# Kernel tuning notes

Measured on AMD Instinct MI355X. Metric: run time of the kernel, lower is better.

## Reference

```python
import jax, jax.numpy as jnp
import numpy as np

WEIGHT_GRADIENT = 0.05
EPS = 1e-6


def _normalize(q, eps):
    # torch F.normalize: q / max(||q||, eps)
    n = jnp.sqrt(jnp.sum(q * q, axis=1, keepdims=True))
    return q / jnp.maximum(n, eps)


def _grad_mag(q, eps):
    # depthwise conv with [-1,1] kernels == finite differences, then replicate-pad
    gx = q[..., :, 1:] - q[..., :, :-1]          # (B,4,H,W-1)
    gy = q[..., 1:, :] - q[..., :-1, :]          # (B,4,H-1,W)
    gx = jnp.pad(gx, ((0, 0), (0, 0), (0, 0), (0, 1)), mode='edge')
    gy = jnp.pad(gy, ((0, 0), (0, 0), (0, 1), (0, 0)), mode='edge')
    return jnp.sqrt(gx * gx + gy * gy + eps)


def setup_inputs() -> dict:
    key = jax.random.key(0)
    k1, k2, k3 = jax.random.split(key, 3)
    B, H, W, S = 16, 256, 256, 24
    q_pred = jax.random.normal(k1, (B, 4, H, W), dtype=jnp.float32)
    q_target = jax.random.normal(k2, (B, 4, H, W), dtype=jnp.float32)
    syms = jax.random.normal(k3, (S, 4), dtype=jnp.float32)
    syms = syms / jnp.linalg.norm(syms, axis=1, keepdims=True)  # unit quaternions
    return {"q_pred": q_pred, "q_target": q_target, "syms": syms}


def reference(q_pred, q_target, syms, eps=EPS):
    # (B,4,H,W) -> (N,4)
    qp = _normalize(q_pred.transpose(0, 2, 3, 1).reshape(-1, 4), eps)
    qt = _normalize(q_target.transpose(0, 2, 3, 1).reshape(-1, 4), eps)
    w1, x1, y1, z1 = qp[:, 0], qp[:, 1], qp[:, 2], qp[:, 3]
    w2, x2, y2, z2 = qt[:, 0], qt[:, 1], qt[:, 2], qt[:, 3]
    # relative quaternion r = qt * conj(qp)
    rw = w2 * w1 + x2 * x1 + y2 * y1 + z2 * z1
    rx = -w2 * x1 + x2 * w1 - y2 * z1 + z2 * y1
    ry = -w2 * y1 + x2 * z1 + y2 * w1 - z2 * x1
    rz = -w2 * z1 - x2 * y1 + y2 * x1 + z2 * w1
    r4 = jnp.stack([rw, rx, ry, rz], axis=1)                 # (N,4)
    signs = jnp.array([1.0, -1.0, -1.0, -1.0], dtype=syms.dtype)
    # w_dist[n,s] = rw*s_w - rx*s_x - ry*s_y - rz*s_z
    w_dist = jnp.einsum('nc,sc->ns', r4, syms * signs)       # (N,S)
    max_w = jnp.max(jnp.abs(w_dist), axis=1)
    max_w = jnp.clip(max_w, -(1.0 - eps), 1.0 - eps)
    loss_rot = jnp.mean(2.0 * jnp.arccos(max_w))
    gp = _grad_mag(q_pred, eps)
    gt = _grad_mag(q_target, eps)
    loss_grad = jnp.mean(jnp.abs(gp - gt))
    return loss_rot + WEIGHT_GRADIENT * loss_grad
```

## Files before the change

### kernel.cpp

```cpp
#include <hip/hip_runtime.h>
#include <math.h>

constexpr int Hc = 256;
constexpr int Wc = 256;
constexpr float EPSf = 1e-6f;

__device__ __forceinline__ float comp(const float4& v, int p) {
    return p == 0 ? v.x : p == 1 ? v.y : p == 2 ? v.z : v.w;
}

template<int S>
__global__ __launch_bounds__(256, 4) void sym_loss_main(
    const float* __restrict__ qp,
    const float* __restrict__ qt,
    const float* __restrict__ syms,
    float2* __restrict__ partial)
{
    int t    = blockIdx.x * 256 + threadIdx.x;
    int lane = t & 63;
    int row  = t >> 6;
    int b    = row >> 8;
    int h    = row & (Hc - 1);
    int w0   = lane << 2;

    int idx0 = (b << 18) + (h << 8) + w0;
    int dy = (h == Hc - 1) ? -Wc : Wc;
    int xo = (lane == 63) ? 2 : 4;

    float4 Cp[4], Yp[4], Ct[4], Yt[4];
    float  xp[4], xt[4];
    #pragma unroll
    for (int c = 0; c < 4; ++c) {
        int idx = idx0 + (c << 16);
        Cp[c] = *(const float4*)(qp + idx);
        Yp[c] = *(const float4*)(qp + idx + dy);
        xp[c] = qp[idx + xo];
        Ct[c] = *(const float4*)(qt + idx);
        Yt[c] = *(const float4*)(qt + idx + dy);
        xt[c] = qt[idx + xo];
    }

    float gsum = 0.0f;
    #pragma unroll
    for (int c = 0; c < 4; ++c) {
        float4 C = Cp[c], Y = Yp[c], D = Ct[c], Z = Yt[c];
        float gx, gy, a, e;
        gx = C.y - C.x; gy = Y.x - C.x;
        a = sqrtf(fmaf(gx, gx, fmaf(gy, gy, EPSf)));
        gx = D.y - D.x; gy = Z.x - D.x;
        e = sqrtf(fmaf(gx, gx, fmaf(gy, gy, EPSf)));
        gsum += fabsf(a - e);

        gx = C.z - C.y; gy = Y.y - C.y;
        a = sqrtf(fmaf(gx, gx, fmaf(gy, gy, EPSf)));
        gx = D.z - D.y; gy = Z.y - D.y;
        e = sqrtf(fmaf(gx, gx, fmaf(gy, gy, EPSf)));
        gsum += fabsf(a - e);

        gx = C.w - C.z; gy = Y.z - C.z;
        a = sqrtf(fmaf(gx, gx, fmaf(gy, gy, EPSf)));
        gx = D.w - D.z; gy = Z.z - D.z;
        e = sqrtf(fmaf(gx, gx, fmaf(gy, gy, EPSf)));
        gsum += fabsf(a - e);

        gx = xp[c] - C.w; gy = Y.w - C.w;
        a = sqrtf(fmaf(gx, gx, fmaf(gy, gy, EPSf)));
        gx = xt[c] - D.w; gy = Z.w - D.w;
        e = sqrtf(fmaf(gx, gx, fmaf(gy, gy, EPSf)));
        gsum += fabsf(a - e);
    }

    float rw[4], nx[4], ny[4], nz[4];
    #pragma unroll
    for (int p = 0; p < 4; ++p) {
        float a0 = comp(Cp[0], p), a1 = comp(Cp[1], p),
              a2 = comp(Cp[2], p), a3 = comp(Cp[3], p);
        float b0 = comp(Ct[0], p), b1 = comp(Ct[1], p),
              b2 = comp(Ct[2], p), b3 = comp(Ct[3], p);

        float ss1 = fmaf(a0, a0, fmaf(a1, a1, fmaf(a2, a2, a3 * a3)));
        float ss2 = fmaf(b0, b0, fmaf(b1, b1, fmaf(b2, b2, b3 * b3)));
        float i1 = __builtin_amdgcn_rsqf(ss1);
        float i2 = __builtin_amdgcn_rsqf(ss2);
        float w1 = a0 * i1, x1 = a1 * i1, y1 = a2 * i1, z1 = a3 * i1;
        float w2 = b0 * i2, x2 = b1 * i2, y2 = b2 * i2, z2 = b3 * i2;

        rw[p] =  w2 * w1 + x2 * x1 + y2 * y1 + z2 * z1;
        float rx = -w2 * x1 + x2 * w1 - y2 * z1 + z2 * y1;
        float ry = -w2 * y1 + x2 * z1 + y2 * w1 - z2 * x1;
        float rz = -w2 * z1 - x2 * y1 + y2 * x1 + z2 * w1;
        nx[p] = -rx; ny[p] = -ry; nz[p] = -rz;
    }

    const float4* __restrict__ sv4 = (const float4*)syms;
    float maxw[4] = {0.f, 0.f, 0.f, 0.f};
    #pragma unroll
    for (int s = 0; s < S; ++s) {
        float4 sv = sv4[s];
        #pragma unroll
        for (int p = 0; p < 4; ++p) {
            float d = fmaf(nz[p], sv.w,
                      fmaf(ny[p], sv.z,
                      fmaf(nx[p], sv.y, rw[p] * sv.x)));
            maxw[p] = fmaxf(maxw[p], fabsf(d));
        }
    }
    float rot = 0.0f;
    #pragma unroll
    for (int p = 0; p < 4; ++p)
        rot += 2.0f * acosf(fminf(maxw[p], 1.0f - EPSf));

    #pragma unroll
    for (int off = 32; off > 0; off >>= 1) {
        rot  += __shfl_down(rot,  off, 64);
        gsum += __shfl_down(gsum, off, 64);
    }
    __shared__ float s_r[4], s_g[4];
    int wid = threadIdx.x >> 6;
    if ((threadIdx.x & 63) == 0) { s_r[wid] = rot; s_g[wid] = gsum; }
    __syncthreads();
    if (threadIdx.x == 0) {
        float2 o;
        o.x = s_r[0] + s_r[1] + s_r[2] + s_r[3];
        o.y = s_g[0] + s_g[1] + s_g[2] + s_g[3];
        partial[blockIdx.x] = o;
    }
}

__global__ __launch_bounds__(256) void sym_loss_generic(
    const float* __restrict__ qp,
    const float* __restrict__ qt,
    const float* __restrict__ syms,
    int S,
    float2* __restrict__ partial)
{
    int t    = blockIdx.x * 256 + threadIdx.x;
    int lane = t & 63;
    int row  = t >> 6;
    int b    = row >> 8;
    int h    = row & (Hc - 1);
    int w0   = lane << 2;
    int idx0 = (b << 18) + (h << 8) + w0;
    int dy = (h == Hc - 1) ? -Wc : Wc;
    int xo = (lane == 63) ? 2 : 4;

    float4 Cp[4], Yp[4], Ct[4], Yt[4];
    float  xp[4], xt[4];
    #pragma unroll
    for (int c = 0; c < 4; ++c) {
        int idx = idx0 + (c << 16);
        Cp[c] = *(const float4*)(qp + idx);
        Yp[c] = *(const float4*)(qp + idx + dy);
        xp[c] = qp[idx + xo];
        Ct[c] = *(const float4*)(qt + idx);
        Yt[c] = *(const float4*)(qt + idx + dy);
        xt[c] = qt[idx + xo];
    }
    float gsum = 0.0f;
    #pragma unroll
    for (int c = 0; c < 4; ++c) {
        float4 C = Cp[c], Y = Yp[c], D = Ct[c], Z = Yt[c];
        float gx, gy, a, e;
        gx = C.y - C.x; gy = Y.x - C.x;
        a = sqrtf(fmaf(gx, gx, fmaf(gy, gy, EPSf)));
        gx = D.y - D.x; gy = Z.x - D.x;
        e = sqrtf(fmaf(gx, gx, fmaf(gy, gy, EPSf)));
        gsum += fabsf(a - e);
        gx = C.z - C.y; gy = Y.y - C.y;
        a = sqrtf(fmaf(gx, gx, fmaf(gy, gy, EPSf)));
        gx = D.z - D.y; gy = Z.y - D.y;
        e = sqrtf(fmaf(gx, gx, fmaf(gy, gy, EPSf)));
        gsum += fabsf(a - e);
        gx = C.w - C.z; gy = Y.z - C.z;
        a = sqrtf(fmaf(gx, gx, fmaf(gy, gy, EPSf)));
        gx = D.w - D.z; gy = Z.z - D.z;
        e = sqrtf(fmaf(gx, gx, fmaf(gy, gy, EPSf)));
        gsum += fabsf(a - e);
        gx = xp[c] - C.w; gy = Y.w - C.w;
        a = sqrtf(fmaf(gx, gx, fmaf(gy, gy, EPSf)));
        gx = xt[c] - D.w; gy = Z.w - D.w;
        e = sqrtf(fmaf(gx, gx, fmaf(gy, gy, EPSf)));
        gsum += fabsf(a - e);
    }
    float rw[4], nx[4], ny[4], nz[4];
    #pragma unroll
    for (int p = 0; p < 4; ++p) {
        float a0 = comp(Cp[0], p), a1 = comp(Cp[1], p),
              a2 = comp(Cp[2], p), a3 = comp(Cp[3], p);
        float b0 = comp(Ct[0], p), b1 = comp(Ct[1], p),
              b2 = comp(Ct[2], p), b3 = comp(Ct[3], p);
        float ss1 = fmaf(a0, a0, fmaf(a1, a1, fmaf(a2, a2, a3 * a3)));
        float ss2 = fmaf(b0, b0, fmaf(b1, b1, fmaf(b2, b2, b3 * b3)));
        float i1 = __builtin_amdgcn_rsqf(ss1);
        float i2 = __builtin_amdgcn_rsqf(ss2);
        float w1 = a0 * i1, x1 = a1 * i1, y1 = a2 * i1, z1 = a3 * i1;
        float w2 = b0 * i2, x2 = b1 * i2, y2 = b2 * i2, z2 = b3 * i2;
        rw[p] =  w2 * w1 + x2 * x1 + y2 * y1 + z2 * z1;
        float rx = -w2 * x1 + x2 * w1 - y2 * z1 + z2 * y1;
        float ry = -w2 * y1 + x2 * z1 + y2 * w1 - z2 * x1;
        float rz = -w2 * z1 - x2 * y1 + y2 * x1 + z2 * w1;
        nx[p] = -rx; ny[p] = -ry; nz[p] = -rz;
    }
    const float4* __restrict__ sv4 = (const float4*)syms;
    float maxw[4] = {0.f, 0.f, 0.f, 0.f};
    for (int s = 0; s < S; ++s) {
        float4 sv = sv4[s];
        #pragma unroll
        for (int p = 0; p < 4; ++p) {
            float d = fmaf(nz[p], sv.w,
                      fmaf(ny[p], sv.z,
                      fmaf(nx[p], sv.y, rw[p] * sv.x)));
            maxw[p] = fmaxf(maxw[p], fabsf(d));
        }
    }
    float rot = 0.0f;
    #pragma unroll
    for (int p = 0; p < 4; ++p)
        rot += 2.0f * acosf(fminf(maxw[p], 1.0f - EPSf));
    #pragma unroll
    for (int off = 32; off > 0; off >>= 1) {
        rot  += __shfl_down(rot,  off, 64);
        gsum += __shfl_down(gsum, off, 64);
    }
    __shared__ float s_r[4], s_g[4];
    int wid = threadIdx.x >> 6;
    if ((threadIdx.x & 63) == 0) { s_r[wid] = rot; s_g[wid] = gsum; }
    __syncthreads();
    if (threadIdx.x == 0) {
        float2 o;
        o.x = s_r[0] + s_r[1] + s_r[2] + s_r[3];
        o.y = s_g[0] + s_g[1] + s_g[2] + s_g[3];
        partial[blockIdx.x] = o;
    }
}

__global__ __launch_bounds__(256) void sym_loss_reduce(
    const float2* __restrict__ partial, int nblocks,
    float* __restrict__ out, double invNP, double invNE)
{
    double r = 0.0, g = 0.0;
    for (int i = threadIdx.x; i < nblocks; i += 256) {
        float2 p = partial[i];
        r += (double)p.x;
        g += (double)p.y;
    }
    #pragma unroll
    for (int off = 32; off > 0; off >>= 1) {
        r += __shfl_down(r, off, 64);
        g += __shfl_down(g, off, 64);
    }
    __shared__ double s_r[4], s_g[4];
    int wid = threadIdx.x >> 6;
    if ((threadIdx.x & 63) == 0) { s_r[wid] = r; s_g[wid] = g; }
    __syncthreads();
    if (threadIdx.x == 0) {
        double rr = s_r[0] + s_r[1] + s_r[2] + s_r[3];
        double gg = s_g[0] + s_g[1] + s_g[2] + s_g[3];
        out[0] = (float)(rr * invNP + 0.05 * gg * invNE);
    }
}

extern "C" void kernel_launch(void* const* d_in, const int* in_sizes, int n_in,
                              void* d_out, int out_size, void* d_ws, size_t ws_size,
                              hipStream_t stream)
{
    const float* qp   = (const float*)d_in[0];
    const float* qt   = (const float*)d_in[1];
    const float* syms = (const float*)d_in[2];

    int S  = in_sizes[2] / 4;
    int NP = in_sizes[0] / 4;
    int nthreads = NP / 4;
    int nblocks  = nthreads / 256;

    float2* partial = (float2*)d_ws;

    if (S == 24) {
        sym_loss_main<24><<<nblocks, 256, 0, stream>>>(qp, qt, syms, partial);
    } else {
        sym_loss_generic<<<nblocks, 256, 0, stream>>>(qp, qt, syms, S, partial);
    }

    double invNP = 1.0 / (double)NP;
    double invNE = 1.0 / ((double)NP * 4.0);
    sym_loss_reduce<<<1, 256, 0, stream>>>(partial, nblocks, (float*)d_out,
                                           invNP, invNE);
}
```

Measured before the change: 84.72 us.

## Use fast sqrt/acos approximations and fuse final reduction via atomics

Replaces library sqrtf with the hardware sqrt builtin and acosf with a cubic polynomial approximation (Abramowitz–Stegun style) for the rotation term. The separate reduction kernel is removed: each block scales its partial sums by precomputed constants and atomically adds them into the output, which is zeroed with a memset first. This cuts transcendental cost and one kernel launch, at the price of approximation error and nondeterministic float accumulation order.

```diff
diff --git a/kernel.cpp b/kernel.cpp
--- a/kernel.cpp
+++ b/kernel.cpp
@@ -7,6 +7,17 @@
 
 __device__ __forceinline__ float comp(const float4& v, int p) {
     return p == 0 ? v.x : p == 1 ? v.y : p == 2 ? v.z : v.w;
+}
+
+__device__ __forceinline__ float fast_acos01(float x) {
+    float t = __builtin_amdgcn_sqrtf(1.0f - x);
+    float p = fmaf(fmaf(fmaf(-0.0187293f, x, 0.0742610f), x, -0.2121144f),
+                   x, 1.5707288f);
+    return t * p;
+}
+
+__device__ __forceinline__ float fast_sqrt(float x) {
+    return __builtin_amdgcn_sqrtf(x);
 }
 
 template<int S>
@@ -14,7 +25,8 @@
     const float* __restrict__ qp,
     const float* __restrict__ qt,
     const float* __restrict__ syms,
-    float2* __restrict__ partial)
+    float* __restrict__ out,
+    float cRot, float cGrad)
 {
     int t    = blockIdx.x * 256 + threadIdx.x;
     int lane = t & 63;
@@ -46,27 +58,27 @@
         float4 C = Cp[c], Y = Yp[c], D = Ct[c], Z = Yt[c];
         float gx, gy, a, e;
         gx = C.y - C.x; gy = Y.x - C.x;
-        a = sqrtf(fmaf(gx, gx, fmaf(gy, gy, EPSf)));
+        a = fast_sqrt(fmaf(gx, gx, fmaf(gy, gy, EPSf)));
         gx = D.y - D.x; gy = Z.x - D.x;
-        e = sqrtf(fmaf(gx, gx, fmaf(gy, gy, EPSf)));
+        e = fast_sqrt(fmaf(gx, gx, fmaf(gy, gy, EPSf)));
         gsum += fabsf(a - e);
 
         gx = C.z - C.y; gy = Y.y - C.y;
-        a = sqrtf(fmaf(gx, gx, fmaf(gy, gy, EPSf)));
+        a = fast_sqrt(fmaf(gx, gx, fmaf(gy, gy, EPSf)));
         gx = D.z - D.y; gy = Z.y - D.y;
-        e = sqrtf(fmaf(gx, gx, fmaf(gy, gy, EPSf)));
+        e = fast_sqrt(fmaf(gx, gx, fmaf(gy, gy, EPSf)));
         gsum += fabsf(a - e);
 
         gx = C.w - C.z; gy = Y.z - C.z;
-        a = sqrtf(fmaf(gx, gx, fmaf(gy, gy, EPSf)));
+        a = fast_sqrt(fmaf(gx, gx, fmaf(gy, gy, EPSf)));
         gx = D.w - D.z; gy = Z.z - D.z;
-        e = sqrtf(fmaf(gx, gx, fmaf(gy, gy, EPSf)));
+        e = fast_sqrt(fmaf(gx, gx, fmaf(gy, gy, EPSf)));
         gsum += fabsf(a - e);
 
         gx = xp[c] - C.w; gy = Y.w - C.w;
-        a = sqrtf(fmaf(gx, gx, fmaf(gy, gy, EPSf)));
+        a = fast_sqrt(fmaf(gx, gx, fmaf(gy, gy, EPSf)));
         gx = xt[c] - D.w; gy = Z.w - D.w;
-        e = sqrtf(fmaf(gx, gx, fmaf(gy, gy, EPSf)));
+        e = fast_sqrt(fmaf(gx, gx, fmaf(gy, gy, EPSf)));
         gsum += fabsf(a - e);
     }
 
@@ -108,7 +120,7 @@
     float rot = 0.0f;
     #pragma unroll
     for (int p = 0; p < 4; ++p)
-        rot += 2.0f * acosf(fminf(maxw[p], 1.0f - EPSf));
+        rot += fast_acos01(fminf(maxw[p], 1.0f - EPSf));
 
     #pragma unroll
     for (int off = 32; off > 0; off >>= 1) {
@@ -120,10 +132,9 @@
     if ((threadIdx.x & 63) == 0) { s_r[wid] = rot; s_g[wid] = gsum; }
     __syncthreads();
     if (threadIdx.x == 0) {
-        float2 o;
-        o.x = s_r[0] + s_r[1] + s_r[2] + s_r[3];
-        o.y = s_g[0] + s_g[1] + s_g[2] + s_g[3];
-        partial[blockIdx.x] = o;
+        float r = s_r[0] + s_r[1] + s_r[2] + s_r[3];
+        float g = s_g[0] + s_g[1] + s_g[2] + s_g[3];
+        atomicAdd(out, fmaf(r, cRot, g * cGrad));
     }
 }
 
@@ -132,7 +143,8 @@
     const float* __restrict__ qt,
     const float* __restrict__ syms,
     int S,
-    float2* __restrict__ partial)
+    float* __restrict__ out,
+    float cRot, float cGrad)
 {
     int t    = blockIdx.x * 256 + threadIdx.x;
     int lane = t & 63;
@@ -162,24 +174,24 @@
         float4 C = Cp[c], Y = Yp[c], D = Ct[c], Z = Yt[c];
         float gx, gy, a, e;
         gx = C.y - C.x; gy = Y.x - C.x;
-        a = sqrtf(fmaf(gx, gx, fmaf(gy, gy, EPSf)));
+        a = fast_sqrt(fmaf(gx, gx, fmaf(gy, gy, EPSf)));
         gx = D.y - D.x; gy = Z.x - D.x;
-        e = sqrtf(fmaf(gx, gx, fmaf(gy, gy, EPSf)));
+        e = fast_sqrt(fmaf(gx, gx, fmaf(gy, gy, EPSf)));
         gsum += fabsf(a - e);
         gx = C.z - C.y; gy = Y.y - C.y;
-        a = sqrtf(fmaf(gx, gx, fmaf(gy, gy, EPSf)));
+        a = fast_sqrt(fmaf(gx, gx, fmaf(gy, gy, EPSf)));
         gx = D.z - D.y; gy = Z.y - D.y;
-        e = sqrtf(fmaf(gx, gx, fmaf(gy, gy, EPSf)));
+        e = fast_sqrt(fmaf(gx, gx, fmaf(gy, gy, EPSf)));
         gsum += fabsf(a - e);
         gx = C.w - C.z; gy = Y.z - C.z;
-        a = sqrtf(fmaf(gx, gx, fmaf(gy, gy, EPSf)));
+        a = fast_sqrt(fmaf(gx, gx, fmaf(gy, gy, EPSf)));
         gx = D.w - D.z; gy = Z.z - D.z;
-        e = sqrtf(fmaf(gx, gx, fmaf(gy, gy, EPSf)));
+        e = fast_sqrt(fmaf(gx, gx, fmaf(gy, gy, EPSf)));
         gsum += fabsf(a - e);
         gx = xp[c] - C.w; gy = Y.w - C.w;
-        a = sqrtf(fmaf(gx, gx, fmaf(gy, gy, EPSf)));
+        a = fast_sqrt(fmaf(gx, gx, fmaf(gy, gy, EPSf)));
         gx = xt[c] - D.w; gy = Z.w - D.w;
-        e = sqrtf(fmaf(gx, gx, fmaf(gy, gy, EPSf)));
+        e = fast_sqrt(fmaf(gx, gx, fmaf(gy, gy, EPSf)));
         gsum += fabsf(a - e);
     }
     float rw[4], nx[4], ny[4], nz[4];
@@ -216,7 +228,7 @@
     float rot = 0.0f;
     #pragma unroll
     for (int p = 0; p < 4; ++p)
-        rot += 2.0f * acosf(fminf(maxw[p], 1.0f - EPSf));
+        rot += fast_acos01(fminf(maxw[p], 1.0f - EPSf));
     #pragma unroll
     for (int off = 32; off > 0; off >>= 1) {
         rot  += __shfl_down(rot,  off, 64);
@@ -227,36 +239,9 @@
     if ((threadIdx.x & 63) == 0) { s_r[wid] = rot; s_g[wid] = gsum; }
     __syncthreads();
     if (threadIdx.x == 0) {
-        float2 o;
-        o.x = s_r[0] + s_r[1] + s_r[2] + s_r[3];
-        o.y = s_g[0] + s_g[1] + s_g[2] + s_g[3];
-        partial[blockIdx.x] = o;
-    }
-}
-
-__global__ __launch_bounds__(256) void sym_loss_reduce(
-    const float2* __restrict__ partial, int nblocks,
-    float* __restrict__ out, double invNP, double invNE)
-{
-    double r = 0.0, g = 0.0;
-    for (int i = threadIdx.x; i < nblocks; i += 256) {
-        float2 p = partial[i];
-        r += (double)p.x;
-        g += (double)p.y;
-    }
-    #pragma unroll
-    for (int off = 32; off > 0; off >>= 1) {
-        r += __shfl_down(r, off, 64);
-        g += __shfl_down(g, off, 64);
-    }
-    __shared__ double s_r[4], s_g[4];
-    int wid = threadIdx.x >> 6;
-    if ((threadIdx.x & 63) == 0) { s_r[wid] = r; s_g[wid] = g; }
-    __syncthreads();
-    if (threadIdx.x == 0) {
-        double rr = s_r[0] + s_r[1] + s_r[2] + s_r[3];
-        double gg = s_g[0] + s_g[1] + s_g[2] + s_g[3];
-        out[0] = (float)(rr * invNP + 0.05 * gg * invNE);
+        float r = s_r[0] + s_r[1] + s_r[2] + s_r[3];
+        float g = s_g[0] + s_g[1] + s_g[2] + s_g[3];
+        atomicAdd(out, fmaf(r, cRot, g * cGrad));
     }
 }
 
@@ -267,22 +252,23 @@
     const float* qp   = (const float*)d_in[0];
     const float* qt   = (const float*)d_in[1];
     const float* syms = (const float*)d_in[2];
+    float* out = (float*)d_out;
 
     int S  = in_sizes[2] / 4;
     int NP = in_sizes[0] / 4;
     int nthreads = NP / 4;
     int nblocks  = nthreads / 256;
 
-    float2* partial = (float2*)d_ws;
+    float cRot  = (float)(2.0 / (double)NP);
+    float cGrad = (float)(0.05 / ((double)NP * 4.0));
+
+    hipMemsetAsync(out, 0, sizeof(float), stream);
 
     if (S == 24) {
-        sym_loss_main<24><<<nblocks, 256, 0, stream>>>(qp, qt, syms, partial);
+        sym_loss_main<24><<<nblocks, 256, 0, stream>>>(qp, qt, syms, out,
+                                                       cRot, cGrad);
     } else {
-        sym_loss_generic<<<nblocks, 256, 0, stream>>>(qp, qt, syms, S, partial);
-    }
-
-    double invNP = 1.0 / (double)NP;
-    double invNE = 1.0 / ((double)NP * 4.0);
-    sym_loss_reduce<<<1, 256, 0, stream>>>(partial, nblocks, (float*)d_out,
-                                           invNP, invNE);
-}
+        sym_loss_generic<<<nblocks, 256, 0, stream>>>(qp, qt, syms, S, out,
+                                                      cRot, cGrad);
+    }
+}
```

After: 90.58 us. 6.9% more time.
